# Kernel optimization log

Hardware: AMD Instinct MI355X
Metric: run time of the kernel (lower is better)

## Reference

```python
import jax, jax.numpy as jnp
import numpy as np

N = 100000      # nodes
E = 1600000     # random edges (self loops added in reference, like add_self_loops)
D_IN = 128
D_OUT = 128
NEG_SLOPE = 0.01  # F.leaky_relu default in the torch source


def setup_inputs() -> dict:
    key = jax.random.key(0)
    k_x, k_e, k_w, k_b, k_a, k_ab = jax.random.split(key, 6)
    x = jax.random.normal(k_x, (N, D_IN), dtype=jnp.float32)
    edge_index = jax.random.randint(k_e, (2, E), 0, N, dtype=jnp.int32)
    # small init scales keep exp(score) in a sane range (torch default init is also small)
    W_lin = jax.random.normal(k_w, (D_OUT, D_IN), dtype=jnp.float32) * 0.05
    b_lin = jax.random.normal(k_b, (D_OUT,), dtype=jnp.float32) * 0.05
    W_att = jax.random.normal(k_a, (1, 2 * D_OUT), dtype=jnp.float32) * 0.05
    b_att = jax.random.normal(k_ab, (1,), dtype=jnp.float32) * 0.05
    return {"x": x, "edge_index": edge_index, "W_lin": W_lin, "b_lin": b_lin,
            "W_att": W_att, "b_att": b_att}


def reference(x, edge_index, W_lin, b_lin, W_att, b_att):
    n = x.shape[0]
    d_out = W_lin.shape[0]
    # h = lin(x), computed ONCE (the torch loop redundantly recomputes it per edge)
    h = x @ W_lin.T + b_lin                      # [N, D_OUT]
    # add self loops (pyg_utils.add_self_loops)
    loops = jnp.arange(n, dtype=edge_index.dtype)
    src = jnp.concatenate([edge_index[0], loops])  # node i (attends over its out-neighbors)
    dst = jnp.concatenate([edge_index[1], loops])  # neighbor j
    # attention([h_i ; h_j]) = h_i . a_i + h_j . a_j + b
    a_i = W_att[0, :d_out]
    a_j = W_att[0, d_out:]
    score = h[src] @ a_i + h[dst] @ a_j + b_att[0]           # [E+N]
    score = jnp.where(score >= 0, score, NEG_SLOPE * score)  # leaky_relu(0.01)
    e = jnp.exp(score)                                        # plain exp, as in source (no max-shift)
    denom = jax.ops.segment_sum(e, src, num_segments=n)       # per-source softmax denominator
    alpha = e / denom[src]                                    # [E+N]
    msg = alpha[:, None] * h[dst]                             # [E+N, D_OUT]
    agg = jax.ops.segment_sum(msg, src, num_segments=n)       # attention_matrix @ h
    return jax.nn.elu(agg)
```

## Files before the change

kernel.cpp:

```cpp
#include <hip/hip_runtime.h>
#include <hip/hip_bf16.h>
#include <stdint.h>

typedef unsigned int uint;
typedef unsigned short ushort;

#define D 128
#define NEG_SLOPE 0.01f
#define BN 128
#define NCHUNK 256
#define KMAX 1024
#define EMAX 4096

using frag_t = __attribute__((ext_vector_type(8))) short;
using f32x4  = __attribute__((ext_vector_type(4))) float;

__device__ __forceinline__ ushort f2bf(float f) {
    __hip_bfloat16 b = __float2bfloat16(f);
    ushort u; __builtin_memcpy(&u, &b, 2); return u;
}
__device__ __forceinline__ float bflo(uint p) { return __uint_as_float(p << 16); }
__device__ __forceinline__ float bfhi(uint p) { return __uint_as_float(p & 0xffff0000u); }

#define LDK 136

__global__ __launch_bounds__(256) void gemm_h(
    const float* __restrict__ x, const float* __restrict__ W,
    const float* __restrict__ bias, const float* __restrict__ Wa,
    const float* __restrict__ ba,
    ushort* __restrict__ h, float* __restrict__ si, float* __restrict__ sj, int n)
{
    __shared__ ushort xs[64 * LDK];
    __shared__ ushort wsh[128 * LDK];
    const int tid  = threadIdx.x;
    const int row0 = blockIdx.x * 64;

    {
        const int r = tid >> 5;
        const int k = (tid & 31) * 4;
#pragma unroll
        for (int i = 0; i < 8; ++i) {
            int lr = r + 8 * i;
            int gr = row0 + lr;
            int cr = gr < n ? gr : (n - 1);
            float4 v = *(const float4*)(x + (size_t)cr * D + k);
            ushort4 u; u.x = f2bf(v.x); u.y = f2bf(v.y); u.z = f2bf(v.z); u.w = f2bf(v.w);
            *(ushort4*)&xs[lr * LDK + k] = u;
        }
#pragma unroll
        for (int i = 0; i < 16; ++i) {
            int lr = r + 8 * i;
            float4 v = *(const float4*)(W + (size_t)lr * D + k);
            ushort4 u; u.x = f2bf(v.x); u.y = f2bf(v.y); u.z = f2bf(v.z); u.w = f2bf(v.w);
            *(ushort4*)&wsh[lr * LDK + k] = u;
        }
    }
    __syncthreads();

    const int wv   = tid >> 6;
    const int lane = tid & 63;
    const int mr   = lane & 15;
    const int qk   = (lane >> 4) * 8;

    f32x4 acc[8] = {};
    const ushort* xrow = xs + (16 * wv + mr) * LDK;
#pragma unroll
    for (int kk = 0; kk < 4; ++kk) {
        frag_t a = *(const frag_t*)(xrow + kk * 32 + qk);
#pragma unroll
        for (int t = 0; t < 8; ++t) {
            frag_t bf = *(const frag_t*)(wsh + (16 * t + mr) * LDK + kk * 32 + qk);
            acc[t] = __builtin_amdgcn_mfma_f32_16x16x32_bf16(a, bf, acc[t], 0, 0, 0);
        }
    }

    const int crow = 16 * wv + (lane >> 4) * 4;
    float pi[4] = {0.f, 0.f, 0.f, 0.f};
    float pj[4] = {0.f, 0.f, 0.f, 0.f};
#pragma unroll
    for (int t = 0; t < 8; ++t) {
        int col = 16 * t + mr;
        float bb = bias[col];
        float av = Wa[col];
        float bv = Wa[D + col];
#pragma unroll
        for (int r = 0; r < 4; ++r) {
            float v = acc[t][r] + bb;
            int grow = row0 + crow + r;
            if (grow < n) h[(size_t)grow * D + col] = f2bf(v);
            pi[r] += v * av;
            pj[r] += v * bv;
        }
    }
#pragma unroll
    for (int o = 1; o < 16; o <<= 1) {
#pragma unroll
        for (int r = 0; r < 4; ++r) {
            pi[r] += __shfl_xor(pi[r], o);
            pj[r] += __shfl_xor(pj[r], o);
        }
    }
    if (mr == 0) {
        float bav = ba[0];
#pragma unroll
        for (int r = 0; r < 4; ++r) {
            int grow = row0 + crow + r;
            if (grow < n) { si[grow] = pi[r] + bav; sj[grow] = pj[r]; }
        }
    }
}

__global__ __launch_bounds__(256) void count_k(
    const int* __restrict__ src, int* __restrict__ counts, int e, int K, int cpb)
{
    __shared__ int hist[KMAX];
    const int c = blockIdx.x;
    for (int b = threadIdx.x; b < K; b += 256) hist[b] = 0;
    __syncthreads();
    const int beg = c * cpb;
    const int end = min(e, beg + cpb);
    for (int i = beg + threadIdx.x; i < end; i += 256)
        atomicAdd(&hist[src[i] >> 7], 1);
    __syncthreads();
    for (int b = threadIdx.x; b < K; b += 256) counts[c * K + b] = hist[b];
}

__global__ __launch_bounds__(256) void scan_chunks(
    const int* __restrict__ counts, int* __restrict__ cbase,
    int* __restrict__ total, int K)
{
    __shared__ int s[NCHUNK];
    const int b = blockIdx.x, t = threadIdx.x;
    int v = counts[t * K + b];
    s[t] = v; __syncthreads();
#pragma unroll
    for (int o = 1; o < NCHUNK; o <<= 1) {
        int tv = (t >= o) ? s[t - o] : 0;
        __syncthreads();
        s[t] += tv;
        __syncthreads();
    }
    cbase[t * K + b] = s[t] - v;
    if (t == NCHUNK - 1) total[b] = s[t];
}

__global__ __launch_bounds__(1024) void scan_buckets(
    const int* __restrict__ total, int* __restrict__ bbase, int K)
{
    __shared__ int s[KMAX];
    const int t = threadIdx.x;
    int v = (t < K) ? total[t] : 0;
    s[t] = v; __syncthreads();
#pragma unroll
    for (int o = 1; o < KMAX; o <<= 1) {
        int tv = (t >= o) ? s[t - o] : 0;
        __syncthreads();
        s[t] += tv;
        __syncthreads();
    }
    if (t < K) bbase[t] = s[t] - v;
}

__global__ __launch_bounds__(256) void fill_k(
    const int* __restrict__ src, const int* __restrict__ dst,
    const int* __restrict__ cbase, const int* __restrict__ bbase,
    uint* __restrict__ barr, int e, int K, int cpb)
{
    __shared__ int cur[KMAX];
    const int c = blockIdx.x;
    for (int b = threadIdx.x; b < K; b += 256)
        cur[b] = cbase[c * K + b] + bbase[b];
    __syncthreads();
    const int beg = c * cpb;
    const int end = min(e, beg + cpb);
    for (int i = beg + threadIdx.x; i < end; i += 256) {
        int s = src[i], d = dst[i];
        int p = atomicAdd(&cur[s >> 7], 1);
        barr[p] = ((uint)(s & (BN - 1)) << 17) | (uint)d;
    }
}

__global__ __launch_bounds__(512) void agg_k(
    const ushort* __restrict__ h, const uint* __restrict__ barr,
    const int* __restrict__ bbase, const int* __restrict__ total,
    const float* __restrict__ si, const float* __restrict__ sj,
    float* __restrict__ out, int n)
{
    __shared__ uint se[EMAX];
    __shared__ int hist[BN];
    __shared__ int base[BN];
    __shared__ int cur[BN];
    const int b   = blockIdx.x;
    const int tid = threadIdx.x;
    const int lane = tid & 63;
    const int wv   = tid >> 6;
    const int node0 = b << 7;

    for (int i = tid; i < BN; i += 512) hist[i] = 0;
    __syncthreads();

    const int ecnt = total[b];
    const uint* eb = barr + bbase[b];

    for (int i = tid; i < ecnt; i += 512)
        atomicAdd(&hist[eb[i] >> 17], 1);
    __syncthreads();

    if (tid < 64) {
        int v0 = hist[2 * tid], v1 = hist[2 * tid + 1];
        int s = v0 + v1;
#pragma unroll
        for (int o = 1; o < 64; o <<= 1) {
            int t = __shfl_up(s, o);
            if (tid >= o) s += t;
        }
        int excl = s - (v0 + v1);
        base[2 * tid] = excl;      cur[2 * tid] = excl;
        base[2 * tid + 1] = excl + v0; cur[2 * tid + 1] = excl + v0;
    }
    __syncthreads();

    for (int i = tid; i < ecnt; i += 512) {
        uint w = eb[i];
        int p = atomicAdd(&cur[w >> 17], 1);
        se[p] = w;
    }
    __syncthreads();

    for (int t = 0; t < 16; ++t) {
        int ls = wv * 16 + t;
        int node = node0 + ls;
        if (node >= n) break;

        float s_i = si[node];
        float sc = s_i + sj[node];
        sc = sc >= 0.f ? sc : NEG_SLOPE * sc;
        float w_ = __expf(sc);
        uint hv = *(const uint*)(h + (size_t)node * D + lane * 2);
        float a0 = w_ * bflo(hv), a1 = w_ * bfhi(hv);
        float denom = w_;

        const int c = hist[ls];
        const uint* seg = se + base[ls];
        int j = 0;
        for (; j + 4 <= c; j += 4) {
            uint w0 = seg[j], w1 = seg[j + 1], w2 = seg[j + 2], w3 = seg[j + 3];
            int d0 = w0 & 0x1FFFF, d1 = w1 & 0x1FFFF;
            int d2 = w2 & 0x1FFFF, d3 = w3 & 0x1FFFF;
            uint g0 = *(const uint*)(h + (size_t)d0 * D + lane * 2);
            uint g1 = *(const uint*)(h + (size_t)d1 * D + lane * 2);
            uint g2 = *(const uint*)(h + (size_t)d2 * D + lane * 2);
            uint g3 = *(const uint*)(h + (size_t)d3 * D + lane * 2);
            float t0 = s_i + sj[d0], t1 = s_i + sj[d1];
            float t2 = s_i + sj[d2], t3 = s_i + sj[d3];
            t0 = t0 >= 0.f ? t0 : NEG_SLOPE * t0;
            t1 = t1 >= 0.f ? t1 : NEG_SLOPE * t1;
            t2 = t2 >= 0.f ? t2 : NEG_SLOPE * t2;
            t3 = t3 >= 0.f ? t3 : NEG_SLOPE * t3;
            float e0 = __expf(t0), e1 = __expf(t1);
            float e2 = __expf(t2), e3 = __expf(t3);
            denom += (e0 + e1) + (e2 + e3);
            a0 += e0 * bflo(g0) + e1 * bflo(g1) + e2 * bflo(g2) + e3 * bflo(g3);
            a1 += e0 * bfhi(g0) + e1 * bfhi(g1) + e2 * bfhi(g2) + e3 * bfhi(g3);
        }
        for (; j < c; ++j) {
            uint w = seg[j];
            int dn = w & 0x1FFFF;
            uint g = *(const uint*)(h + (size_t)dn * D + lane * 2);
            float ts = s_i + sj[dn];
            ts = ts >= 0.f ? ts : NEG_SLOPE * ts;
            float we = __expf(ts);
            denom += we;
            a0 += we * bflo(g);
            a1 += we * bfhi(g);
        }

        float inv = 1.f / denom;
        a0 *= inv; a1 *= inv;
        a0 = a0 > 0.f ? a0 : expm1f(a0);
        a1 = a1 > 0.f ? a1 : expm1f(a1);
        *(float2*)(out + (size_t)node * D + lane * 2) = make_float2(a0, a1);
    }
}

extern "C" void kernel_launch(void* const* d_in, const int* in_sizes, int n_in,
                              void* d_out, int out_size, void* d_ws, size_t ws_size,
                              hipStream_t stream)
{
    const float* x  = (const float*)d_in[0];
    const int*   ei = (const int*)  d_in[1];
    const float* Wl = (const float*)d_in[2];
    const float* bl = (const float*)d_in[3];
    const float* Wa = (const float*)d_in[4];
    const float* ba = (const float*)d_in[5];
    const int n = in_sizes[0] / D;
    const int e = in_sizes[1] / 2;
    const int* src = ei;
    const int* dst = ei + e;

    const int K   = (n + BN - 1) / BN;
    const int cpb = (e + NCHUNK - 1) / NCHUNK;

    char* w = (char*)d_ws;
    size_t off = 0;
    ushort* h      = (ushort*)(w + off); off += (size_t)n * D * 2;
    float*  si     = (float*) (w + off); off += (size_t)n * 4;
    float*  sj     = (float*) (w + off); off += (size_t)n * 4;
    int*    counts = (int*)   (w + off); off += (size_t)NCHUNK * K * 4;
    int*    cbase  = (int*)   (w + off); off += (size_t)NCHUNK * K * 4;
    int*    total  = (int*)   (w + off); off += (size_t)K * 4;
    int*    bbase  = (int*)   (w + off); off += (size_t)K * 4;
    uint*   barr   = (uint*)  (w + off); off += (size_t)e * 4;

    gemm_h      <<<(n + 63) / 64, 256, 0, stream>>>(x, Wl, bl, Wa, ba, h, si, sj, n);
    count_k     <<<NCHUNK,        256, 0, stream>>>(src, counts, e, K, cpb);
    scan_chunks <<<K,             256, 0, stream>>>(counts, cbase, total, K);
    scan_buckets<<<1,            1024, 0, stream>>>(total, bbase, K);
    fill_k      <<<NCHUNK,        256, 0, stream>>>(src, dst, cbase, bbase, barr, e, K, cpb);
    agg_k       <<<K,             512, 0, stream>>>(h, barr, bbase, total, si, sj, (float*)d_out, n);
}
```

Measured before the change: 249.7 us.

## Precompute edge weights in fill pass and gather two edges per wave

fill_k now computes each edge's leaky-relu/exp attention weight and stores it next to the packed source/destination index as an 8-byte record. This removes the random sj gathers and exp work from the aggregation loop. agg_k splits each wave into two half-waves that handle alternate edges, each lane loading 8 bytes of h, and merges the halves with a cross-lane shuffle before normalising and applying elu. NCHUNK doubles to 512 so the counting and fill passes run more blocks. In exchange, the bucket array and LDS staging double in size, and fill_k now does random reads of si and sj.

Result: slower. 255.3 us (+2.3%).

```diff
diff --git a/kernel.cpp b/kernel.cpp
--- a/kernel.cpp
+++ b/kernel.cpp
@@ -8,7 +8,7 @@
 #define D 128
 #define NEG_SLOPE 0.01f
 #define BN 128
-#define NCHUNK 256
+#define NCHUNK 512
 #define KMAX 1024
 #define EMAX 4096
 
@@ -125,7 +125,7 @@
     for (int b = threadIdx.x; b < K; b += 256) counts[c * K + b] = hist[b];
 }
 
-__global__ __launch_bounds__(256) void scan_chunks(
+__global__ __launch_bounds__(NCHUNK) void scan_chunks(
     const int* __restrict__ counts, int* __restrict__ cbase,
     int* __restrict__ total, int K)
 {
@@ -163,8 +163,9 @@
 
 __global__ __launch_bounds__(256) void fill_k(
     const int* __restrict__ src, const int* __restrict__ dst,
+    const float* __restrict__ si, const float* __restrict__ sj,
     const int* __restrict__ cbase, const int* __restrict__ bbase,
-    uint* __restrict__ barr, int e, int K, int cpb)
+    uint2* __restrict__ barr, int e, int K, int cpb)
 {
     __shared__ int cur[KMAX];
     const int c = blockIdx.x;
@@ -175,35 +176,41 @@
     const int end = min(e, beg + cpb);
     for (int i = beg + threadIdx.x; i < end; i += 256) {
         int s = src[i], d = dst[i];
+        float sc = si[s] + sj[d];
+        sc = sc >= 0.f ? sc : NEG_SLOPE * sc;
+        float w = __expf(sc);
         int p = atomicAdd(&cur[s >> 7], 1);
-        barr[p] = ((uint)(s & (BN - 1)) << 17) | (uint)d;
+        barr[p] = make_uint2(((uint)(s & (BN - 1)) << 17) | (uint)d,
+                             __float_as_uint(w));
     }
 }
 
 __global__ __launch_bounds__(512) void agg_k(
-    const ushort* __restrict__ h, const uint* __restrict__ barr,
+    const ushort* __restrict__ h, const uint2* __restrict__ barr,
     const int* __restrict__ bbase, const int* __restrict__ total,
     const float* __restrict__ si, const float* __restrict__ sj,
     float* __restrict__ out, int n)
 {
-    __shared__ uint se[EMAX];
+    __shared__ uint2 se[EMAX];
     __shared__ int hist[BN];
     __shared__ int base[BN];
     __shared__ int cur[BN];
-    const int b   = blockIdx.x;
-    const int tid = threadIdx.x;
+    const int b    = blockIdx.x;
+    const int tid  = threadIdx.x;
     const int lane = tid & 63;
     const int wv   = tid >> 6;
+    const int hw   = lane >> 5;
+    const int l32  = lane & 31;
     const int node0 = b << 7;
 
     for (int i = tid; i < BN; i += 512) hist[i] = 0;
     __syncthreads();
 
     const int ecnt = total[b];
-    const uint* eb = barr + bbase[b];
+    const uint2* eb = barr + bbase[b];
 
     for (int i = tid; i < ecnt; i += 512)
-        atomicAdd(&hist[eb[i] >> 17], 1);
+        atomicAdd(&hist[eb[i].x >> 17], 1);
     __syncthreads();
 
     if (tid < 64) {
@@ -215,71 +222,79 @@
             if (tid >= o) s += t;
         }
         int excl = s - (v0 + v1);
-        base[2 * tid] = excl;      cur[2 * tid] = excl;
+        base[2 * tid] = excl;          cur[2 * tid] = excl;
         base[2 * tid + 1] = excl + v0; cur[2 * tid + 1] = excl + v0;
     }
     __syncthreads();
 
     for (int i = tid; i < ecnt; i += 512) {
-        uint w = eb[i];
-        int p = atomicAdd(&cur[w >> 17], 1);
-        se[p] = w;
-    }
-    __syncthreads();
+        uint2 r = eb[i];
+        int p = atomicAdd(&cur[r.x >> 17], 1);
+        se[p] = r;
+    }
+    __syncthreads();
+
+    const char* hp = (const char*)h + l32 * 8;
 
     for (int t = 0; t < 16; ++t) {
         int ls = wv * 16 + t;
         int node = node0 + ls;
         if (node >= n) break;
 
-        float s_i = si[node];
-        float sc = s_i + sj[node];
-        sc = sc >= 0.f ? sc : NEG_SLOPE * sc;
-        float w_ = __expf(sc);
-        uint hv = *(const uint*)(h + (size_t)node * D + lane * 2);
-        float a0 = w_ * bflo(hv), a1 = w_ * bfhi(hv);
-        float denom = w_;
-
         const int c = hist[ls];
-        const uint* seg = se + base[ls];
+        const uint2* seg = se + base[ls];
+        float a0 = 0.f, a1 = 0.f, a2 = 0.f, a3 = 0.f, den = 0.f;
+
         int j = 0;
-        for (; j + 4 <= c; j += 4) {
-            uint w0 = seg[j], w1 = seg[j + 1], w2 = seg[j + 2], w3 = seg[j + 3];
-            int d0 = w0 & 0x1FFFF, d1 = w1 & 0x1FFFF;
-            int d2 = w2 & 0x1FFFF, d3 = w3 & 0x1FFFF;
-            uint g0 = *(const uint*)(h + (size_t)d0 * D + lane * 2);
-            uint g1 = *(const uint*)(h + (size_t)d1 * D + lane * 2);
-            uint g2 = *(const uint*)(h + (size_t)d2 * D + lane * 2);
-            uint g3 = *(const uint*)(h + (size_t)d3 * D + lane * 2);
-            float t0 = s_i + sj[d0], t1 = s_i + sj[d1];
-            float t2 = s_i + sj[d2], t3 = s_i + sj[d3];
-            t0 = t0 >= 0.f ? t0 : NEG_SLOPE * t0;
-            t1 = t1 >= 0.f ? t1 : NEG_SLOPE * t1;
-            t2 = t2 >= 0.f ? t2 : NEG_SLOPE * t2;
-            t3 = t3 >= 0.f ? t3 : NEG_SLOPE * t3;
-            float e0 = __expf(t0), e1 = __expf(t1);
-            float e2 = __expf(t2), e3 = __expf(t3);
-            denom += (e0 + e1) + (e2 + e3);
-            a0 += e0 * bflo(g0) + e1 * bflo(g1) + e2 * bflo(g2) + e3 * bflo(g3);
-            a1 += e0 * bfhi(g0) + e1 * bfhi(g1) + e2 * bfhi(g2) + e3 * bfhi(g3);
-        }
-        for (; j < c; ++j) {
-            uint w = seg[j];
-            int dn = w & 0x1FFFF;
-            uint g = *(const uint*)(h + (size_t)dn * D + lane * 2);
-            float ts = s_i + sj[dn];
-            ts = ts >= 0.f ? ts : NEG_SLOPE * ts;
-            float we = __expf(ts);
-            denom += we;
-            a0 += we * bflo(g);
-            a1 += we * bfhi(g);
-        }
-
-        float inv = 1.f / denom;
-        a0 *= inv; a1 *= inv;
-        a0 = a0 > 0.f ? a0 : expm1f(a0);
-        a1 = a1 > 0.f ? a1 : expm1f(a1);
-        *(float2*)(out + (size_t)node * D + lane * 2) = make_float2(a0, a1);
+        for (; j + 8 <= c; j += 8) {
+            uint2 r0 = seg[j + 0 + hw], r1 = seg[j + 2 + hw];
+            uint2 r2 = seg[j + 4 + hw], r3 = seg[j + 6 + hw];
+            uint2 g0 = *(const uint2*)(hp + ((size_t)(r0.x & 0x1FFFF) << 8));
+            uint2 g1 = *(const uint2*)(hp + ((size_t)(r1.x & 0x1FFFF) << 8));
+            uint2 g2 = *(const uint2*)(hp + ((size_t)(r2.x & 0x1FFFF) << 8));
+            uint2 g3 = *(const uint2*)(hp + ((size_t)(r3.x & 0x1FFFF) << 8));
+            float w0 = __uint_as_float(r0.y), w1 = __uint_as_float(r1.y);
+            float w2 = __uint_as_float(r2.y), w3 = __uint_as_float(r3.y);
+            den += (w0 + w1) + (w2 + w3);
+            a0 += w0 * bflo(g0.x); a1 += w0 * bfhi(g0.x);
+            a2 += w0 * bflo(g0.y); a3 += w0 * bfhi(g0.y);
+            a0 += w1 * bflo(g1.x); a1 += w1 * bfhi(g1.x);
+            a2 += w1 * bflo(g1.y); a3 += w1 * bfhi(g1.y);
+            a0 += w2 * bflo(g2.x); a1 += w2 * bfhi(g2.x);
+            a2 += w2 * bflo(g2.y); a3 += w2 * bfhi(g2.y);
+            a0 += w3 * bflo(g3.x); a1 += w3 * bfhi(g3.x);
+            a2 += w3 * bflo(g3.y); a3 += w3 * bfhi(g3.y);
+        }
+        for (; j < c; j += 2) {
+            int idx = j + hw;
+            uint2 r = seg[idx < c ? idx : j];
+            float w = idx < c ? __uint_as_float(r.y) : 0.f;
+            uint2 g = *(const uint2*)(hp + ((size_t)(r.x & 0x1FFFF) << 8));
+            den += w;
+            a0 += w * bflo(g.x); a1 += w * bfhi(g.x);
+            a2 += w * bflo(g.y); a3 += w * bfhi(g.y);
+        }
+
+        a0 += __shfl_xor(a0, 32); a1 += __shfl_xor(a1, 32);
+        a2 += __shfl_xor(a2, 32); a3 += __shfl_xor(a3, 32);
+        den += __shfl_xor(den, 32);
+
+        if (hw == 0) {
+            float sc = si[node] + sj[node];
+            sc = sc >= 0.f ? sc : NEG_SLOPE * sc;
+            float w_ = __expf(sc);
+            uint2 hv = *(const uint2*)((const char*)h + ((size_t)node << 8) + l32 * 8);
+            a0 += w_ * bflo(hv.x); a1 += w_ * bfhi(hv.x);
+            a2 += w_ * bflo(hv.y); a3 += w_ * bfhi(hv.y);
+            den += w_;
+            float inv = 1.f / den;
+            a0 *= inv; a1 *= inv; a2 *= inv; a3 *= inv;
+            a0 = a0 > 0.f ? a0 : expm1f(a0);
+            a1 = a1 > 0.f ? a1 : expm1f(a1);
+            a2 = a2 > 0.f ? a2 : expm1f(a2);
+            a3 = a3 > 0.f ? a3 : expm1f(a3);
+            *(float4*)(out + ((size_t)node << 7) + l32 * 4) = make_float4(a0, a1, a2, a3);
+        }
     }
 }
 
@@ -309,13 +324,13 @@
     int*    counts = (int*)   (w + off); off += (size_t)NCHUNK * K * 4;
     int*    cbase  = (int*)   (w + off); off += (size_t)NCHUNK * K * 4;
     int*    total  = (int*)   (w + off); off += (size_t)K * 4;
-    int*    bbase  = (int*)   (w + off); off += (size_t)K * 4;
-    uint*   barr   = (uint*)  (w + off); off += (size_t)e * 4;
+    int*    bbase  = (int*)   (w + off); off += (size_t)K * 4 + 8;
+    uint2*  barr   = (uint2*) (w + off); off += (size_t)e * 8;
 
     gemm_h      <<<(n + 63) / 64, 256, 0, stream>>>(x, Wl, bl, Wa, ba, h, si, sj, n);
     count_k     <<<NCHUNK,        256, 0, stream>>>(src, counts, e, K, cpb);
-    scan_chunks <<<K,             256, 0, stream>>>(counts, cbase, total, K);
+    scan_chunks <<<K,          NCHUNK, 0, stream>>>(counts, cbase, total, K);
     scan_buckets<<<1,            1024, 0, stream>>>(total, bbase, K);
-    fill_k      <<<NCHUNK,        256, 0, stream>>>(src, dst, cbase, bbase, barr, e, K, cpb);
+    fill_k      <<<NCHUNK,        256, 0, stream>>>(src, dst, si, sj, cbase, bbase, barr, e, K, cpb);
     agg_k       <<<K,             512, 0, stream>>>(h, barr, bbase, total, si, sj, (float*)d_out, n);
 }
```
